# Optimization experiments

Hardware: AMD Instinct MI355X
Metric: run time of the kernel (lower is better)

The kernel has to match this reference:

```python
import jax, jax.numpy as jnp
import numpy as np

IGNORE_LABEL_ID = -100
GRID = 40                 # grid_width
PATH = 6                  # path_token_id
SP_W = 10.0               # spatial_penalty_weight
CONN_W = 5.0              # connectivity_weight
SEQ = GRID * GRID         # 1600
BIG = SEQ                 # sentinel larger than any flat index


def _spatial_penalty(pred):
    """Vectorized version of spatial_connectivity_loss's per-batch python loop.
    For each predicted path token, find the NEXT path token in flat order and
    penalize Manhattan jumps > 1. pred: [B, SEQ] int."""
    B = pred.shape[0]
    mask = pred == PATH                                   # [B,S]
    idx = jnp.arange(SEQ, dtype=jnp.int32)
    cand = jnp.where(mask, idx[None, :], BIG)
    # nxt[b,i] = smallest path index >= i (reverse cumulative min)
    nxt = jax.lax.cummin(cand, axis=1, reverse=True)
    # next path index strictly after i
    nxt_after = jnp.concatenate([nxt[:, 1:], jnp.full((B, 1), BIG, nxt.dtype)], axis=1)
    valid = mask & (nxt_after < BIG)                      # pairs (i, next)
    p2 = jnp.minimum(nxt_after, SEQ - 1)                  # keep indices in-range
    r1, c1 = idx // GRID, idx % GRID
    r2, c2 = p2 // GRID, p2 % GRID
    dist = jnp.abs(r1[None, :] - r2) + jnp.abs(c1[None, :] - c2)
    pen = jnp.where(valid & (dist > 1), (dist - 1).astype(jnp.float32) * SP_W, 0.0)
    return pen.sum() / B


def _connectivity_penalty(pred):
    """Parallel connected-component labeling (min-label propagation) replacing
    the CPU flood fill. pred: [B, SEQ] int."""
    B = pred.shape[0]
    mask = pred.reshape(B, GRID, GRID) == PATH
    idx = jnp.arange(SEQ, dtype=jnp.int32).reshape(GRID, GRID)
    lab0 = jnp.where(mask, idx[None], BIG)

    def prop(lab):
        p = jnp.pad(lab, ((0, 0), (1, 1), (1, 1)), constant_values=BIG)
        nmin = jnp.minimum(jnp.minimum(p[:, :-2, 1:-1], p[:, 2:, 1:-1]),
                           jnp.minimum(p[:, 1:-1, :-2], p[:, 1:-1, 2:]))
        return jnp.where(mask, jnp.minimum(lab, nmin), BIG)

    def cond(st):
        return st[1]

    def body(st):
        lab, _ = st
        new = prop(lab)
        return (new, jnp.any(new != lab))

    lab, _ = jax.lax.while_loop(cond, body, (lab0, jnp.array(True)))
    # a component is counted once at its minimal (root) cell
    comp = (mask & (lab == idx[None])).sum(axis=(1, 2))
    pen = jnp.where(comp > 1, (comp - 1).astype(jnp.float32) * CONN_W, 0.0)
    return pen.sum() / B


def setup_inputs() -> dict:
    key = jax.random.key(0)
    k1, k2, k3, k4, k5 = jax.random.split(key, 5)
    B, S, V = 1024, SEQ, 32
    return {
        "logits": jax.random.normal(k1, (B, S, V), dtype=jnp.float32),
        "labels": jax.random.randint(k2, (B, S), 0, V).astype(jnp.int64),
        "q_halt_logits": jax.random.normal(k3, (B,), dtype=jnp.float32),
        "halted": jax.random.randint(k4, (B,), 0, 2).astype(bool),
        "steps": jax.random.randint(k5, (B,), 0, 16).astype(jnp.int32),
    }


def reference(logits, labels, q_halt_logits, halted, steps):
    # halted/steps feed no-grad metrics only; loss math below matches ACTLossHead.
    mask = labels != IGNORE_LABEL_ID                       # [B,S]
    loss_counts = mask.sum(-1)
    loss_divisor = jnp.maximum(loss_counts, 1)[:, None].astype(logits.dtype)

    pred = jnp.argmax(logits, axis=-1)                     # [B,S]
    is_correct = mask & (pred == labels)
    seq_is_correct = is_correct.sum(-1) == loss_counts     # [B] bool

    # softmax cross entropy with ignore_index, per token
    logp = jax.nn.log_softmax(logits, axis=-1)
    safe_labels = jnp.maximum(labels, 0)
    ce = -jnp.take_along_axis(logp, safe_labels[..., None], axis=-1)[..., 0]
    ce = jnp.where(mask, ce, 0.0)
    lm_loss = (ce / loss_divisor).sum()

    # BCE-with-logits, reduction='sum'
    t = seq_is_correct.astype(logits.dtype)
    x = q_halt_logits
    q_halt_loss = (jnp.maximum(x, 0) - x * t + jnp.log1p(jnp.exp(-jnp.abs(x)))).sum()

    spatial_loss = _spatial_penalty(pred)
    connectivity_loss = _connectivity_penalty(pred)

    total_loss = lm_loss + 0.5 * q_halt_loss + spatial_loss + connectivity_loss
    return total_loss
```

## Files before the change

### kernel.cpp

```cpp
#include <hip/hip_runtime.h>
#include <cstdint>

#define GRIDW   40
#define SEQ     1600
#define NVOCAB  32
#define PATH_ID 6
#define IGNORE_ID (-100)
#define NWORDS  25
#define BLK     256

__global__ __launch_bounds__(BLK) void act_loss_kernel(
    const float* __restrict__ logits,
    const int*   __restrict__ labels,
    const float* __restrict__ qhalt,
    float*       __restrict__ out,
    int B)
{
    const int b   = blockIdx.x;
    const int tid = threadIdx.x;

    __shared__ uint8_t  path[SEQ];
    __shared__ uint16_t lab[SEQ];
    __shared__ uint16_t pos[SEQ];
    __shared__ uint64_t words[NWORDS];
    __shared__ int      offs[NWORDS + 1];
    __shared__ int      npath_s;
    __shared__ float    red_f[BLK];
    __shared__ int      red_i[BLK];
    __shared__ int      red_j[BLK];
    __shared__ int      changed;
    __shared__ float    part_a;

    float ce_sum = 0.0f;
    int   cnt = 0, cor = 0;

    const float* base  = logits + (size_t)b * SEQ * NVOCAB;
    const int*   lbase = labels + (size_t)b * SEQ;

    for (int i = tid; i < SEQ; i += BLK) {
        const float4* p4 = (const float4*)(base + (size_t)i * NVOCAB);
        float x[NVOCAB];
#pragma unroll
        for (int j = 0; j < 8; ++j) {
            float4 v = p4[j];
            x[4*j+0] = v.x; x[4*j+1] = v.y; x[4*j+2] = v.z; x[4*j+3] = v.w;
        }
        int lbl = lbase[i];

        float m = x[0]; int arg = 0;
#pragma unroll
        for (int j = 1; j < NVOCAB; ++j) {
            if (x[j] > m) { m = x[j]; arg = j; }
        }
        float s = 0.0f;
#pragma unroll
        for (int j = 0; j < NVOCAB; ++j) s += __expf(x[j] - m);
        float lse = m + __logf(s);

        bool msk  = (lbl != IGNORE_ID);
        int  slbl = (lbl < 0) ? 0 : lbl;
        float xl = 0.0f;
#pragma unroll
        for (int j = 0; j < NVOCAB; ++j) xl = (j == slbl) ? x[j] : xl;

        ce_sum += msk ? (lse - xl) : 0.0f;
        cnt    += msk ? 1 : 0;
        cor    += (msk && arg == lbl) ? 1 : 0;
        path[i] = (arg == PATH_ID) ? 1 : 0;
    }
    __syncthreads();

    red_f[tid] = ce_sum; red_i[tid] = cnt; red_j[tid] = cor;
    __syncthreads();
    for (int s = BLK / 2; s > 0; s >>= 1) {
        if (tid < s) {
            red_f[tid] += red_f[tid + s];
            red_i[tid] += red_i[tid + s];
            red_j[tid] += red_j[tid + s];
        }
        __syncthreads();
    }
    if (tid == 0) {
        float ce_tot = red_f[0];
        int   c_tot  = red_i[0];
        int   k_tot  = red_j[0];
        float lm = ce_tot / (float)max(c_tot, 1);
        float t  = (k_tot == c_tot) ? 1.0f : 0.0f;
        float xq = qhalt[b];
        float bce = fmaxf(xq, 0.0f) - xq * t + log1pf(expf(-fabsf(xq)));
        part_a = lm + 0.5f * bce;
    }
    __syncthreads();

    if (tid < NWORDS) {
        uint64_t w = 0;
        int basei = tid * 64;
#pragma unroll 8
        for (int k = 0; k < 64; ++k)
            w |= ((uint64_t)path[basei + k]) << k;
        words[tid] = w;
    }
    __syncthreads();
    if (tid == 0) {
        int o = 0;
        for (int t2 = 0; t2 < NWORDS; ++t2) { offs[t2] = o; o += __popcll(words[t2]); }
        offs[NWORDS] = o;
        npath_s = o;
    }
    __syncthreads();
    if (tid < NWORDS) {
        int o = offs[tid];
        uint64_t w = words[tid];
        int basei = tid * 64;
        while (w) {
            int k = __ffsll((unsigned long long)w) - 1;
            pos[o++] = (uint16_t)(basei + k);
            w &= (w - 1);
        }
    }
    __syncthreads();

    const int np = npath_s;
    int sp_units = 0;
    for (int q = tid; q + 1 < np; q += BLK) {
        int i = pos[q], j = pos[q + 1];
        int dist = abs(i / GRIDW - j / GRIDW) + abs(i % GRIDW - j % GRIDW);
        if (dist > 1) sp_units += dist - 1;
    }

    for (int i = tid; i < SEQ; i += BLK)
        lab[i] = path[i] ? (uint16_t)i : (uint16_t)0xFFFF;
    __syncthreads();

    for (;;) {
        if (tid == 0) changed = 0;
        __syncthreads();
        int local = 0;
        for (int i = tid; i < SEQ; i += BLK) {
            if (!path[i]) continue;
            int r = i / GRIDW, c = i % GRIDW;
            uint16_t v = lab[i];
            uint16_t nm = v;
            if (r > 0)          { uint16_t u = lab[i - GRIDW]; nm = (u < nm) ? u : nm; }
            if (r < GRIDW - 1)  { uint16_t u = lab[i + GRIDW]; nm = (u < nm) ? u : nm; }
            if (c > 0)          { uint16_t u = lab[i - 1];     nm = (u < nm) ? u : nm; }
            if (c < GRIDW - 1)  { uint16_t u = lab[i + 1];     nm = (u < nm) ? u : nm; }
            if (nm < v) { lab[i] = nm; local = 1; }
        }
        if (local) changed = 1;
        __syncthreads();
        if (!changed) break;
    }

    int comp = 0;
    for (int i = tid; i < SEQ; i += BLK)
        comp += (path[i] && lab[i] == (uint16_t)i) ? 1 : 0;

    red_i[tid] = sp_units; red_j[tid] = comp;
    __syncthreads();
    for (int s = BLK / 2; s > 0; s >>= 1) {
        if (tid < s) {
            red_i[tid] += red_i[tid + s];
            red_j[tid] += red_j[tid + s];
        }
        __syncthreads();
    }

    if (tid == 0) {
        int sp_tot   = red_i[0];
        int comp_tot = red_j[0];
        int conn_units = (comp_tot > 1) ? (comp_tot - 1) : 0;
        float total = part_a +
                      ((float)sp_tot * 10.0f + (float)conn_units * 5.0f) / (float)B;
        atomicAdd(out, total);
    }
}

extern "C" void kernel_launch(void* const* d_in, const int* in_sizes, int n_in,
                              void* d_out, int out_size, void* d_ws, size_t ws_size,
                              hipStream_t stream) {
    const float* logits = (const float*)d_in[0];
    const int*   labels = (const int*)d_in[1];
    const float* qhalt  = (const float*)d_in[2];
    float* out = (float*)d_out;
    const int B = in_sizes[2];

    hipMemsetAsync(out, 0, (size_t)out_size * sizeof(float), stream);
    act_loss_kernel<<<dim3(B), dim3(BLK), 0, stream>>>(logits, labels, qhalt, out, B);
}
```

Before: 305.7 us.

## Stage logits through LDS with direct global-to-LDS loads and rotated reads

```diff
diff --git a/kernel.cpp b/kernel.cpp
--- a/kernel.cpp
+++ b/kernel.cpp
@@ -8,6 +8,10 @@
 #define IGNORE_ID (-100)
 #define NWORDS  25
 #define BLK     256
+#define CHUNK   256
+
+#define AS1 __attribute__((address_space(1)))
+#define AS3 __attribute__((address_space(3)))
 
 __global__ __launch_bounds__(BLK) void act_loss_kernel(
     const float* __restrict__ logits,
@@ -16,18 +20,17 @@
     float*       __restrict__ out,
     int B)
 {
-    const int b   = blockIdx.x;
-    const int tid = threadIdx.x;
-
+    const int b    = blockIdx.x;
+    const int tid  = threadIdx.x;
+    const int wave = tid >> 6;
+    const int lane = tid & 63;
+
+    __shared__ uint32_t chunk[CHUNK * NVOCAB];
     __shared__ uint8_t  path[SEQ];
-    __shared__ uint16_t lab[SEQ];
-    __shared__ uint16_t pos[SEQ];
-    __shared__ uint64_t words[NWORDS];
-    __shared__ int      offs[NWORDS + 1];
-    __shared__ int      npath_s;
     __shared__ float    red_f[BLK];
     __shared__ int      red_i[BLK];
     __shared__ int      red_j[BLK];
+    __shared__ int      npath_s;
     __shared__ int      changed;
     __shared__ float    part_a;
 
@@ -37,38 +40,53 @@
     const float* base  = logits + (size_t)b * SEQ * NVOCAB;
     const int*   lbase = labels + (size_t)b * SEQ;
 
-    for (int i = tid; i < SEQ; i += BLK) {
-        const float4* p4 = (const float4*)(base + (size_t)i * NVOCAB);
-        float x[NVOCAB];
+    for (int c0 = 0; c0 < SEQ; c0 += CHUNK) {
+        const int Tc   = min(CHUNK, SEQ - c0);
+        const int nseg = Tc >> 3;
+        const float4* gsrc = (const float4*)(base + (size_t)c0 * NVOCAB);
+
+        for (int seg = wave; seg < nseg; seg += 4) {
+            const float4* src = gsrc + seg * 64 + lane;
+            __builtin_amdgcn_global_load_lds((const AS1 void*)src,
+                                             (AS3 void*)&chunk[seg * 256],
+                                             16, 0, 0);
+        }
+        __syncthreads();
+
+        if (tid < Tc) {
+            const int i = c0 + tid;
+            const float* row = (const float*)&chunk[tid * NVOCAB];
+            float x[NVOCAB];
 #pragma unroll
-        for (int j = 0; j < 8; ++j) {
-            float4 v = p4[j];
-            x[4*j+0] = v.x; x[4*j+1] = v.y; x[4*j+2] = v.z; x[4*j+3] = v.w;
-        }
-        int lbl = lbase[i];
-
-        float m = x[0]; int arg = 0;
+            for (int j = 0; j < NVOCAB; ++j)
+                x[j] = row[(j + tid) & (NVOCAB - 1)];
+
+            const int  lbl  = lbase[i];
+            const bool msk  = (lbl != IGNORE_ID);
+            const int  slbl = (lbl < 0) ? 0 : lbl;
+
+            float m = -3.0e38f, xl = 0.0f;
+            int   arg = NVOCAB;
 #pragma unroll
-        for (int j = 1; j < NVOCAB; ++j) {
-            if (x[j] > m) { m = x[j]; arg = j; }
-        }
-        float s = 0.0f;
+            for (int j = 0; j < NVOCAB; ++j) {
+                const int v = (j + tid) & (NVOCAB - 1);
+                const bool take = (x[j] > m) || (x[j] == m && v < arg);
+                if (take) { m = x[j]; arg = v; }
+                xl = (v == slbl) ? x[j] : xl;
+            }
+            float s = 0.0f;
 #pragma unroll
-        for (int j = 0; j < NVOCAB; ++j) s += __expf(x[j] - m);
-        float lse = m + __logf(s);
-
-        bool msk  = (lbl != IGNORE_ID);
-        int  slbl = (lbl < 0) ? 0 : lbl;
-        float xl = 0.0f;
-#pragma unroll
-        for (int j = 0; j < NVOCAB; ++j) xl = (j == slbl) ? x[j] : xl;
-
-        ce_sum += msk ? (lse - xl) : 0.0f;
-        cnt    += msk ? 1 : 0;
-        cor    += (msk && arg == lbl) ? 1 : 0;
-        path[i] = (arg == PATH_ID) ? 1 : 0;
-    }
-    __syncthreads();
+            for (int j = 0; j < NVOCAB; ++j)
+                s += __expf(x[j] - m);
+            const float lse = m + __logf(s);
+
+            ce_sum += msk ? (lse - xl) : 0.0f;
+            cnt    += msk ? 1 : 0;
+            cor    += (msk && arg == lbl) ? 1 : 0;
+            path[i] = (arg == PATH_ID) ? 1 : 0;
+        }
+        __syncthreads();
+    }
 
     red_f[tid] = ce_sum; red_i[tid] = cnt; red_j[tid] = cor;
     __syncthreads();
@@ -90,6 +108,11 @@
         float bce = fmaxf(xq, 0.0f) - xq * t + log1pf(expf(-fabsf(xq)));
         part_a = lm + 0.5f * bce;
     }
+
+    uint16_t* lab   = (uint16_t*)chunk;
+    uint16_t* pos   = (uint16_t*)chunk + SEQ;
+    uint64_t* words = (uint64_t*)&chunk[1600];
+    int*      offs  = (int*)&chunk[1652];
     __syncthreads();
 
     if (tid < NWORDS) {
@@ -104,7 +127,6 @@
     if (tid == 0) {
         int o = 0;
         for (int t2 = 0; t2 < NWORDS; ++t2) { offs[t2] = o; o += __popcll(words[t2]); }
-        offs[NWORDS] = o;
         npath_s = o;
     }
     __syncthreads();
```

Measured after the change: 312.0 us. +2.1%, slower.

## Split each row's vocab across 8 lanes with shuffle reductions for coalesced loads

Applied to the files above, without the earlier changes.

```diff
diff --git a/kernel.cpp b/kernel.cpp
--- a/kernel.cpp
+++ b/kernel.cpp
@@ -16,57 +16,71 @@
     float*       __restrict__ out,
     int B)
 {
-    const int b   = blockIdx.x;
-    const int tid = threadIdx.x;
+    const int b    = blockIdx.x;
+    const int tid  = threadIdx.x;
+    const int wave = tid >> 6;
+    const int lane = tid & 63;
+    const int grp  = lane >> 3;
+    const int q    = lane & 7;
 
     __shared__ uint8_t  path[SEQ];
     __shared__ uint16_t lab[SEQ];
     __shared__ uint16_t pos[SEQ];
     __shared__ uint64_t words[NWORDS];
     __shared__ int      offs[NWORDS + 1];
-    __shared__ int      npath_s;
     __shared__ float    red_f[BLK];
     __shared__ int      red_i[BLK];
     __shared__ int      red_j[BLK];
+    __shared__ int      npath_s;
     __shared__ int      changed;
     __shared__ float    part_a;
 
     float ce_sum = 0.0f;
     int   cnt = 0, cor = 0;
 
-    const float* base  = logits + (size_t)b * SEQ * NVOCAB;
-    const int*   lbase = labels + (size_t)b * SEQ;
-
-    for (int i = tid; i < SEQ; i += BLK) {
-        const float4* p4 = (const float4*)(base + (size_t)i * NVOCAB);
-        float x[NVOCAB];
+    const float4* base4 = (const float4*)(logits + (size_t)b * SEQ * NVOCAB);
+    const int*    lbase = labels + (size_t)b * SEQ;
+
+#pragma unroll 2
+    for (int it = 0; it < SEQ / 32; ++it) {
+        const int   t = it * 32 + wave * 8 + grp;
+        const float4 v = base4[it * 256 + wave * 64 + lane];
+        const int   lbl = lbase[t];
+
+        float m = v.x; int a = q * 4;
+        if (v.y > m) { m = v.y; a = q * 4 + 1; }
+        if (v.z > m) { m = v.z; a = q * 4 + 2; }
+        if (v.w > m) { m = v.w; a = q * 4 + 3; }
+
 #pragma unroll
-        for (int j = 0; j < 8; ++j) {
-            float4 v = p4[j];
-            x[4*j+0] = v.x; x[4*j+1] = v.y; x[4*j+2] = v.z; x[4*j+3] = v.w;
-        }
-        int lbl = lbase[i];
-
-        float m = x[0]; int arg = 0;
+        for (int d = 1; d <= 4; d <<= 1) {
+            float om = __shfl_xor(m, d);
+            int   oa = __shfl_xor(a, d);
+            if (om > m || (om == m && oa < a)) { m = om; a = oa; }
+        }
+
+        const int  slbl = (lbl < 0) ? 0 : lbl;
+        float s  = __expf(v.x - m) + __expf(v.y - m)
+                 + __expf(v.z - m) + __expf(v.w - m);
+        float xl = 0.0f;
+        xl = (q * 4 + 0 == slbl) ? v.x : xl;
+        xl = (q * 4 + 1 == slbl) ? v.y : xl;
+        xl = (q * 4 + 2 == slbl) ? v.z : xl;
+        xl = (q * 4 + 3 == slbl) ? v.w : xl;
 #pragma unroll
-        for (int j = 1; j < NVOCAB; ++j) {
-            if (x[j] > m) { m = x[j]; arg = j; }
-        }
-        float s = 0.0f;
-#pragma unroll
-        for (int j = 0; j < NVOCAB; ++j) s += __expf(x[j] - m);
-        float lse = m + __logf(s);
-
-        bool msk  = (lbl != IGNORE_ID);
-        int  slbl = (lbl < 0) ? 0 : lbl;
-        float xl = 0.0f;
-#pragma unroll
-        for (int j = 0; j < NVOCAB; ++j) xl = (j == slbl) ? x[j] : xl;
-
-        ce_sum += msk ? (lse - xl) : 0.0f;
-        cnt    += msk ? 1 : 0;
-        cor    += (msk && arg == lbl) ? 1 : 0;
-        path[i] = (arg == PATH_ID) ? 1 : 0;
+        for (int d = 1; d <= 4; d <<= 1) {
+            s  += __shfl_xor(s, d);
+            xl += __shfl_xor(xl, d);
+        }
+
+        if (q == 0) {
+            const bool msk = (lbl != IGNORE_ID);
+            const float ce = (m + __logf(s)) - xl;
+            ce_sum += msk ? ce : 0.0f;
+            cnt    += msk ? 1 : 0;
+            cor    += (msk && a == lbl) ? 1 : 0;
+            path[t] = (a == PATH_ID) ? 1 : 0;
+        }
     }
     __syncthreads();
 
@@ -104,7 +118,6 @@
     if (tid == 0) {
         int o = 0;
         for (int t2 = 0; t2 < NWORDS; ++t2) { offs[t2] = o; o += __popcll(words[t2]); }
-        offs[NWORDS] = o;
         npath_s = o;
     }
     __syncthreads();
@@ -122,8 +135,8 @@
 
     const int np = npath_s;
     int sp_units = 0;
-    for (int q = tid; q + 1 < np; q += BLK) {
-        int i = pos[q], j = pos[q + 1];
+    for (int p = tid; p + 1 < np; p += BLK) {
+        int i = pos[p], j = pos[p + 1];
         int dist = abs(i / GRIDW - j / GRIDW) + abs(i % GRIDW - j % GRIDW);
         if (dist > 1) sp_units += dist - 1;
     }
```

After: 312.6 us. 1.02x slower.
